# Kernel tuning notes

Measured on AMD Instinct MI355X. Metric: run time of the kernel, lower is better.

The kernel has to match this reference:

```python
import jax, jax.numpy as jnp
import numpy as np

OCC_THR = 0.5      # occupancy_threshold
RADIUS = 1.0       # point_match_radius
BOX = 30.0         # spatial extent so radius-1 matching is non-trivial
N_PRED = 8192
N_TRUE = 4096


def setup_inputs() -> dict:
    key = jax.random.key(0)
    k1, k2, k3, k4 = jax.random.split(key, 4)
    pred_xyz = jax.random.uniform(k1, (N_PRED, 3), dtype=jnp.float32) * BOX
    pred_p = jax.random.uniform(k2, (N_PRED, 1), dtype=jnp.float32)
    true_xyz = jax.random.uniform(k3, (N_TRUE, 3), dtype=jnp.float32) * BOX
    true_p = jax.random.uniform(k4, (N_TRUE, 1), dtype=jnp.float32)
    return {
        "pred_cloud": jnp.concatenate([pred_xyz, pred_p], axis=1),
        "true_cloud": jnp.concatenate([true_xyz, true_p], axis=1),
    }


def reference(pred_cloud, true_cloud):
    INF = jnp.float32(jnp.inf)
    pred_valid = pred_cloud[:, 3] >= OCC_THR          # [N_pred] occupancy filter
    true_valid = true_cloud[:, 3] >= OCC_THR          # [N_true]
    px, tx = pred_cloud[:, :3], true_cloud[:, :3]
    pp, tp = pred_cloud[:, 3], true_cloud[:, 3]

    # Pairwise Euclidean distances [N_true, N_pred]; invalid preds and
    # out-of-radius pairs are set to +inf (mirrors cdist + valid_mask in torch).
    d2 = jnp.sum((tx[:, None, :] - px[None, :, :]) ** 2, axis=-1)
    dists = jnp.sqrt(d2)
    dists = jnp.where(pred_valid[None, :] & (dists <= RADIUS), dists, INF)

    n_pred = px.shape[0]

    def step(carry, row):
        suppressed, sum_dist, cnt, sum_sq = carry
        d_row, t_ok, t_prob = row
        d = jnp.where(suppressed, INF, d_row)
        j = jnp.argmin(d)
        dmin = d[j]
        matched = t_ok & jnp.isfinite(dmin)
        suppressed = suppressed.at[j].set(suppressed[j] | matched)
        sum_dist = sum_dist + jnp.where(matched, dmin, 0.0)
        sum_sq = sum_sq + jnp.where(matched, (t_prob - pp[j]) ** 2, 0.0)
        cnt = cnt + matched.astype(jnp.int32)
        return (suppressed, sum_dist, cnt, sum_sq), None

    init = (jnp.zeros((n_pred,), bool), jnp.float32(0.0), jnp.int32(0), jnp.float32(0.0))
    (_, sum_dist, cnt, sum_sq), _ = jax.lax.scan(step, init, (dists, true_valid, tp))

    num_true = jnp.sum(true_valid).astype(jnp.float32)
    cnt_f = cnt.astype(jnp.float32)
    unmatched = num_true - cnt_f
    has = cnt > 0
    denom = jnp.maximum(cnt_f, 1.0)
    spatial_error = RADIUS * 10.0 * unmatched + jnp.where(has, sum_dist / denom, 0.0)
    prob_error = unmatched + jnp.where(has, sum_sq / denom, 0.0)
    return spatial_error + prob_error
```

## Files before the change

### kernel.cpp

```cpp
#include <hip/hip_runtime.h>
#include <stdint.h>

typedef unsigned int u32;
typedef unsigned long long u64;

#define OCC_THR   0.5f
#define RADIUS_F  1.0f
#define D2_PRE    1.000002f
#define MAXP      8192
#define BTHREADS  256
#define TB        4
#define K2_THREADS 512
#define PER       8
#define CAP       16

__global__ void __launch_bounds__(BTHREADS) k_build(
    const float4* __restrict__ pred, const float4* __restrict__ tru,
    int n_pred, int n_true,
    u32* __restrict__ counts, u64* __restrict__ rowmin,
    u64* __restrict__ crows)
{
    __shared__ float4 st[TB];
    __shared__ u32    lcnt[TB];
    __shared__ u64    lmin[TB];
    __shared__ u64    lrow[TB][CAP];

    const int tid = threadIdx.x;
    const int ti0 = blockIdx.x * TB;

    if (tid < TB) {
        int i = ti0 + tid;
        st[tid]   = (i < n_true) ? tru[i] : make_float4(1e30f, 1e30f, 1e30f, 0.0f);
        lcnt[tid] = 0u;
        lmin[tid] = ~0ull;
    }
    __syncthreads();

    const float4 q0 = st[0], q1 = st[1], q2 = st[2], q3 = st[3];

#define TEST_T(t, q) {                                                       \
        float dx = (q).x - px, dy = (q).y - p.y, dz = (q).z - p.z;           \
        float d2 = dx*dx + dy*dy + dz*dz;                                    \
        if (d2 <= D2_PRE) {                                                  \
            float d = sqrtf(d2);                                             \
            if (d <= RADIUS_F) {          \
                u64 key = ((u64)__float_as_uint(d) << 32) | (u32)j;          \
                u32 slot = atomicAdd(&lcnt[t], 1u);                          \
                if (slot < (u32)CAP) lrow[t][slot] = key;                    \
                atomicMin(&lmin[t], key);                                    \
            }                                                                \
        }                                                                    \
    }

    for (int j = tid; j < n_pred; j += BTHREADS) {
        const float4 p = pred[j];
        const float px = (p.w >= OCC_THR) ? p.x : 1e30f;
        TEST_T(0, q0) TEST_T(1, q1) TEST_T(2, q2) TEST_T(3, q3)
    }
#undef TEST_T
    __syncthreads();

    if (tid < TB) {
        int i = ti0 + tid;
        if (i < n_true) {
            u32 c = lcnt[tid];
            if (c > (u32)CAP) c = (u32)CAP;
            counts[i] = c;
            rowmin[i] = lmin[tid];
        }
    }
    if (tid < TB * CAP) {
        int t = tid >> 4, s = tid & 15;
        int i = ti0 + t;
        u32 c = lcnt[t];
        if (c > (u32)CAP) c = (u32)CAP;
        if (i < n_true && (u32)s < c)
            crows[(size_t)i * CAP + s] = lrow[t][s];
    }
}

__global__ void __launch_bounds__(K2_THREADS) k_match(
    const float4* __restrict__ pred, const float4* __restrict__ tru,
    int n_true,
    const u32* __restrict__ counts,
    const u64* __restrict__ rowmin,
    const u64* __restrict__ crows,
    float* __restrict__ out)
{
    __shared__ u32   s_owner[MAXP];
    __shared__ int   s_flag;
    __shared__ int   s_numtrue;
    __shared__ float s_rd[8], s_rq[8];
    __shared__ int   s_rc[8];

    const int tid = threadIdx.x;
    if (tid == 0) s_numtrue = 0;
    for (int j = tid; j < MAXP; j += K2_THREADS) s_owner[j] = 0xFFFFFFFFu;

    float tp[PER]; u32 curj[PER]; float dist[PER]; u64 prop[PER];
    u64 pre[PER]; u32 eff[PER];
    u32 srch = 0;
    int myvalid = 0;

#define INIT_K(k) {                                                          \
        const int i = tid * PER + k;                                         \
        tp[k] = 0.0f; curj[k] = 0xFFFFFFFFu; dist[k] = 0.0f;                 \
        pre[k] = ~0ull; eff[k] = 0;                                          \
        if (i < n_true) {                                                    \
            float4 q = tru[i];                                               \
            tp[k] = q.w;                                                     \
            if (q.w >= OCC_THR) {                                            \
                myvalid++;                                                   \
                u32 c = counts[i];                                           \
                eff[k] = (c > (u32)CAP) ? (u32)CAP : c;                      \
                if (eff[k] > 0u) {                                           \
                    srch |= (1u << k);                                       \
                    pre[k] = rowmin[i];          \
                }                                                            \
            }                                                                \
        }                                                                    \
    }
    INIT_K(0) INIT_K(1) INIT_K(2) INIT_K(3)
    INIT_K(4) INIT_K(5) INIT_K(6) INIT_K(7)
#undef INIT_K

    if (myvalid) atomicAdd(&s_numtrue, myvalid);
    __syncthreads();

    for (;;) {
        if (tid == 0) s_flag = 0;
        __syncthreads();

#define PROP_K(k) {                                                          \
        prop[k] = ~0ull;                                                     \
        if (srch & (1u << k)) {                                              \
            const u32 i = (u32)(tid * PER + k);                              \
            u64 best;                                                        \
            if (pre[k] != ~0ull) { best = pre[k]; pre[k] = ~0ull; }          \
            else {                                                           \
                const u64* row = crows + (size_t)i * CAP;                    \
                best = ~0ull;                                                \
                for (u32 kk = 0; kk < eff[k]; ++kk) {                        \
                    u64 cd = row[kk];                                        \
                    if (s_owner[(u32)cd] > i && cd < best) best = cd;        \
                }                                                            \
            }                                                                \
            if (best != ~0ull) {                                             \
                atomicMin(&s_owner[(u32)best], i);                           \
                prop[k] = best;                                              \
            } else {                                                         \
                srch &= ~(1u << k);        \
            }                                                                \
        }                                                                    \
    }
        PROP_K(0) PROP_K(1) PROP_K(2) PROP_K(3)
        PROP_K(4) PROP_K(5) PROP_K(6) PROP_K(7)
#undef PROP_K
        __syncthreads();

        bool any = false;
#define ACC_K(k) {                                                           \
        const u32 i = (u32)(tid * PER + k);                                  \
        if (prop[k] != ~0ull) {                                              \
            const u32 j = (u32)prop[k];                                      \
            if (s_owner[j] == i) {                       \
                curj[k] = j;                                                 \
                dist[k] = __uint_as_float((u32)(prop[k] >> 32));             \
                srch &= ~(1u << k);                                          \
            } else { any = true; }                    \
        } else if (curj[k] != 0xFFFFFFFFu) {                                 \
            if (s_owner[curj[k]] != i) {           \
                curj[k] = 0xFFFFFFFFu;                                       \
                srch |= (1u << k);                                           \
                any = true;                                                  \
            }                                                                \
        }                                                                    \
    }
        ACC_K(0) ACC_K(1) ACC_K(2) ACC_K(3)
        ACC_K(4) ACC_K(5) ACC_K(6) ACC_K(7)
#undef ACC_K

        if (any) s_flag = 1;
        __syncthreads();
        if (!s_flag) break;
    }

    float sd = 0.0f, sq = 0.0f; int cnt = 0;
#define SUM_K(k) {                                                           \
        if (curj[k] != 0xFFFFFFFFu) {                                        \
            sd += dist[k];                                                   \
            float pw = pred[curj[k]].w;                                      \
            float df = tp[k] - pw;                                           \
            sq += df * df;                                                   \
            cnt++;                                                           \
        }                                                                    \
    }
    SUM_K(0) SUM_K(1) SUM_K(2) SUM_K(3)
    SUM_K(4) SUM_K(5) SUM_K(6) SUM_K(7)
#undef SUM_K

    for (int o = 32; o > 0; o >>= 1) {
        sd  += __shfl_down(sd,  o, 64);
        sq  += __shfl_down(sq,  o, 64);
        cnt += __shfl_down(cnt, o, 64);
    }
    const int wave = tid >> 6;
    if ((tid & 63) == 0) { s_rd[wave] = sd; s_rq[wave] = sq; s_rc[wave] = cnt; }
    __syncthreads();

    if (tid == 0) {
        float tsd = 0.0f, tsq = 0.0f; int tc = 0;
        for (int w = 0; w < K2_THREADS / 64; ++w) { tsd += s_rd[w]; tsq += s_rq[w]; tc += s_rc[w]; }
        float num_true  = (float)s_numtrue;
        float cnt_f     = (float)tc;
        float unmatched = num_true - cnt_f;
        float denom     = fmaxf(cnt_f, 1.0f);
        bool  has       = tc > 0;
        float spatial   = RADIUS_F * 10.0f * unmatched + (has ? tsd / denom : 0.0f);
        float prob      = unmatched + (has ? tsq / denom : 0.0f);
        out[0] = spatial + prob;
    }
}

extern "C" void kernel_launch(void* const* d_in, const int* in_sizes, int n_in,
                              void* d_out, int out_size, void* d_ws, size_t ws_size,
                              hipStream_t stream) {
    const float4* pred = (const float4*)d_in[0];
    const float4* tru  = (const float4*)d_in[1];
    const int n_pred = in_sizes[0] / 4;
    const int n_true = in_sizes[1] / 4;

    size_t counts_bytes = (size_t)n_true * sizeof(u32);
    size_t off_rmin  = (counts_bytes + 255) & ~(size_t)255;
    size_t off_crows = (off_rmin + (size_t)n_true * 8 + 255) & ~(size_t)255;

    u32* counts = (u32*)d_ws;
    u64* rowmin = (u64*)((char*)d_ws + off_rmin);
    u64* crows  = (u64*)((char*)d_ws + off_crows);

    k_build<<<(n_true + TB - 1) / TB, BTHREADS, 0, stream>>>(
        pred, tru, n_pred, n_true, counts, rowmin, crows);
    k_match<<<1, K2_THREADS, 0, stream>>>(
        pred, tru, n_true, counts, rowmin, crows, (float*)d_out);
}
```

Baseline: 38.47 us.

## Fuse build and match kernels via global flags, pre-sort candidate rows

Merges the candidate-build kernel and the single-block matching kernel into one launch. Block 0 spin-waits on per-block release flags before running the matching phase, and clears the flags when it finishes. Each row's candidate list is insertion-sorted in shared memory, so the first entry doubles as the row minimum (the separate rowmin atomics go away) and the re-proposal scan can stop at the first unowned candidate. The block size rises to 512. This removes a launch boundary, but every block now reserves the 32KB owner array, which may lower occupancy in the build phase. It also relies on all blocks making forward progress while block 0 spins.

```diff
diff --git a/kernel.cpp b/kernel.cpp
--- a/kernel.cpp
+++ b/kernel.cpp
@@ -8,31 +8,35 @@
 #define RADIUS_F  1.0f
 #define D2_PRE    1.000002f
 #define MAXP      8192
-#define BTHREADS  256
+#define THREADS   512
 #define TB        4
-#define K2_THREADS 512
 #define PER       8
 #define CAP       16
-
-__global__ void __launch_bounds__(BTHREADS) k_build(
+#define MAGIC     0x9E3779B9u
+
+__global__ void __launch_bounds__(THREADS) k_fused(
     const float4* __restrict__ pred, const float4* __restrict__ tru,
-    int n_pred, int n_true,
-    u32* __restrict__ counts, u64* __restrict__ rowmin,
-    u64* __restrict__ crows)
+    int n_pred, int n_true, int nblocks,
+    u32* __restrict__ counts, u64* __restrict__ crows,
+    u32* __restrict__ gflags, float* __restrict__ out)
 {
     __shared__ float4 st[TB];
     __shared__ u32    lcnt[TB];
-    __shared__ u64    lmin[TB];
     __shared__ u64    lrow[TB][CAP];
+    __shared__ u32    s_owner[MAXP];
+    __shared__ int    s_flag;
+    __shared__ int    s_numtrue;
+    __shared__ float  s_rd[8], s_rq[8];
+    __shared__ int    s_rc[8];
 
     const int tid = threadIdx.x;
-    const int ti0 = blockIdx.x * TB;
+    const int bid = blockIdx.x;
+    const int ti0 = bid * TB;
 
     if (tid < TB) {
         int i = ti0 + tid;
         st[tid]   = (i < n_true) ? tru[i] : make_float4(1e30f, 1e30f, 1e30f, 0.0f);
         lcnt[tid] = 0u;
-        lmin[tid] = ~0ull;
     }
     __syncthreads();
 
@@ -47,12 +51,10 @@
                 u64 key = ((u64)__float_as_uint(d) << 32) | (u32)j;          \
                 u32 slot = atomicAdd(&lcnt[t], 1u);                          \
                 if (slot < (u32)CAP) lrow[t][slot] = key;                    \
-                atomicMin(&lmin[t], key);                                    \
-            }                                                                \
-        }                                                                    \
-    }
-
-    for (int j = tid; j < n_pred; j += BTHREADS) {
+            }                                                                \
+        }                                                                    \
+    }
+    for (int j = tid; j < n_pred; j += THREADS) {
         const float4 p = pred[j];
         const float px = (p.w >= OCC_THR) ? p.x : 1e30f;
         TEST_T(0, q0) TEST_T(1, q1) TEST_T(2, q2) TEST_T(3, q3)
@@ -65,37 +67,39 @@
         if (i < n_true) {
             u32 c = lcnt[tid];
             if (c > (u32)CAP) c = (u32)CAP;
+            for (u32 a = 1; a < c; ++a) {
+                u64 v = lrow[tid][a];
+                int b = (int)a - 1;
+                while (b >= 0 && lrow[tid][b] > v) { lrow[tid][b+1] = lrow[tid][b]; --b; }
+                lrow[tid][b+1] = v;
+            }
             counts[i] = c;
-            rowmin[i] = lmin[tid];
+            for (u32 s = 0; s < c; ++s)
+                crows[(size_t)i * CAP + s] = lrow[tid][s];
         }
     }
-    if (tid < TB * CAP) {
-        int t = tid >> 4, s = tid & 15;
-        int i = ti0 + t;
-        u32 c = lcnt[t];
-        if (c > (u32)CAP) c = (u32)CAP;
-        if (i < n_true && (u32)s < c)
-            crows[(size_t)i * CAP + s] = lrow[t][s];
-    }
-}
-
-__global__ void __launch_bounds__(K2_THREADS) k_match(
-    const float4* __restrict__ pred, const float4* __restrict__ tru,
-    int n_true,
-    const u32* __restrict__ counts,
-    const u64* __restrict__ rowmin,
-    const u64* __restrict__ crows,
-    float* __restrict__ out)
-{
-    __shared__ u32   s_owner[MAXP];
-    __shared__ int   s_flag;
-    __shared__ int   s_numtrue;
-    __shared__ float s_rd[8], s_rq[8];
-    __shared__ int   s_rc[8];
-
-    const int tid = threadIdx.x;
+    __syncthreads();
+    if (tid == 0) {
+        __threadfence();
+        __hip_atomic_store(&gflags[bid], MAGIC, __ATOMIC_RELEASE,
+                           __HIP_MEMORY_SCOPE_AGENT);
+    }
+
+    if (bid != 0) return;
+
+    for (int f = tid; f < nblocks; f += THREADS) {
+        int guard = 0;
+        while (__hip_atomic_load(&gflags[f], __ATOMIC_ACQUIRE,
+                                 __HIP_MEMORY_SCOPE_AGENT) != MAGIC) {
+            __builtin_amdgcn_s_sleep(2);
+            if (++guard > 4000000) break;
+        }
+    }
+    __syncthreads();
+    __threadfence();
+
     if (tid == 0) s_numtrue = 0;
-    for (int j = tid; j < MAXP; j += K2_THREADS) s_owner[j] = 0xFFFFFFFFu;
+    for (int j = tid; j < MAXP; j += THREADS) s_owner[j] = 0xFFFFFFFFu;
 
     float tp[PER]; u32 curj[PER]; float dist[PER]; u64 prop[PER];
     u64 pre[PER]; u32 eff[PER];
@@ -115,7 +119,7 @@
                 eff[k] = (c > (u32)CAP) ? (u32)CAP : c;                      \
                 if (eff[k] > 0u) {                                           \
                     srch |= (1u << k);                                       \
-                    pre[k] = rowmin[i];          \
+                    pre[k] = crows[(size_t)i * CAP];     \
                 }                                                            \
             }                                                                \
         }                                                                    \
@@ -142,8 +146,8 @@
                 best = ~0ull;                                                \
                 for (u32 kk = 0; kk < eff[k]; ++kk) {                        \
                     u64 cd = row[kk];                                        \
-                    if (s_owner[(u32)cd] > i && cd < best) best = cd;        \
-                }                                                            \
+                    if (s_owner[(u32)cd] > i) { best = cd; break; }          \
+                }                \
             }                                                                \
             if (best != ~0ull) {                                             \
                 atomicMin(&s_owner[(u32)best], i);                           \
@@ -210,7 +214,7 @@
 
     if (tid == 0) {
         float tsd = 0.0f, tsq = 0.0f; int tc = 0;
-        for (int w = 0; w < K2_THREADS / 64; ++w) { tsd += s_rd[w]; tsq += s_rq[w]; tc += s_rc[w]; }
+        for (int w = 0; w < THREADS / 64; ++w) { tsd += s_rd[w]; tsq += s_rq[w]; tc += s_rc[w]; }
         float num_true  = (float)s_numtrue;
         float cnt_f     = (float)tc;
         float unmatched = num_true - cnt_f;
@@ -220,6 +224,11 @@
         float prob      = unmatched + (has ? tsq / denom : 0.0f);
         out[0] = spatial + prob;
     }
+    __syncthreads();
+
+    for (int f = tid; f < nblocks; f += THREADS)
+        __hip_atomic_store(&gflags[f], 0u, __ATOMIC_RELAXED,
+                           __HIP_MEMORY_SCOPE_AGENT);
 }
 
 extern "C" void kernel_launch(void* const* d_in, const int* in_sizes, int n_in,
@@ -230,16 +239,16 @@
     const int n_pred = in_sizes[0] / 4;
     const int n_true = in_sizes[1] / 4;
 
+    const int nblocks = (n_true + TB - 1) / TB;
+
     size_t counts_bytes = (size_t)n_true * sizeof(u32);
-    size_t off_rmin  = (counts_bytes + 255) & ~(size_t)255;
-    size_t off_crows = (off_rmin + (size_t)n_true * 8 + 255) & ~(size_t)255;
+    size_t off_crows = (counts_bytes + 255) & ~(size_t)255;
+    size_t off_flags = (off_crows + (size_t)n_true * CAP * 8 + 255) & ~(size_t)255;
 
     u32* counts = (u32*)d_ws;
-    u64* rowmin = (u64*)((char*)d_ws + off_rmin);
     u64* crows  = (u64*)((char*)d_ws + off_crows);
-
-    k_build<<<(n_true + TB - 1) / TB, BTHREADS, 0, stream>>>(
-        pred, tru, n_pred, n_true, counts, rowmin, crows);
-    k_match<<<1, K2_THREADS, 0, stream>>>(
-        pred, tru, n_true, counts, rowmin, crows, (float*)d_out);
+    u32* gflags = (u32*)((char*)d_ws + off_flags);
+
+    k_fused<<<nblocks, THREADS, 0, stream>>>(pred, tru, n_pred, n_true, nblocks,
+                                             counts, crows, gflags, (float*)d_out);
 }
```

After: 67.50 us. 75.5% more time.
